# Performance work log

Hardware: AMD Instinct MI355X
Metric: run time of the kernel (lower is better)

Reference implementation:

```python
import jax, jax.numpy as jnp
import numpy as np

H = 16          # attention_head_num
DH = 64         # attention_head_size
D = H * DH      # out_dim / model dim
SIZE_PER_HEAD = 64  # scaling denominator (init arg, used as sqrt divisor)


def setup_inputs() -> dict:
    key = jax.random.key(0)
    ks = jax.random.split(key, 12)
    B, S = 2, 2048
    scale = 1.0 / np.sqrt(D)
    inp = {
        "qx": jax.random.normal(ks[0], (B, S, D), dtype=jnp.float32),
        "kx": jax.random.normal(ks[1], (B, S, D), dtype=jnp.float32),
        "vx": jax.random.normal(ks[2], (B, S, D), dtype=jnp.float32),
        "Wq": jax.random.normal(ks[3], (D, D), dtype=jnp.float32) * scale,
        "bq": jnp.zeros((D,), dtype=jnp.float32),
        "Wk": jax.random.normal(ks[4], (D, D), dtype=jnp.float32) * scale,
        "bk": jnp.zeros((D,), dtype=jnp.float32),
        "Wv": jax.random.normal(ks[5], (D, D), dtype=jnp.float32) * scale,
        "bv": jnp.zeros((D,), dtype=jnp.float32),
        "Wo": jax.random.normal(ks[6], (D, D), dtype=jnp.float32) * scale,
        "bo": jnp.zeros((D,), dtype=jnp.float32),
    }
    return inp


def reference(qx, kx, vx, Wq, bq, Wk, bk, Wv, bv, Wo, bo):
    B, Sq, _ = qx.shape
    Sk = kx.shape[1]
    # QKV projections
    q = qx @ Wq + bq  # [B,Sq,D]
    k = kx @ Wk + bk  # [B,Sk,D]
    v = vx @ Wv + bv  # [B,Sk,D]
    # split heads -> [B,H,S,DH]
    q = q.reshape(B, Sq, H, DH).transpose(0, 2, 1, 3)
    k = k.reshape(B, Sk, H, DH).transpose(0, 2, 1, 3)
    v = v.reshape(B, Sk, H, DH).transpose(0, 2, 1, 3)
    # scores [B,H,Sq,Sk]; NOTE: original divides by sqrt(size_per_head)
    scores = jnp.einsum("bhqd,bhkd->bhqk", q, k) / jnp.sqrt(
        jnp.asarray(SIZE_PER_HEAD, dtype=q.dtype)
    )
    probs = jax.nn.softmax(scores, axis=-1)
    ctx = jnp.einsum("bhqk,bhkd->bhqd", probs, v)  # [B,H,Sq,DH]
    ctx = ctx.transpose(0, 2, 1, 3).reshape(B, Sq, D)
    return ctx @ Wo + bo
```

## Files before the change

### kernel.cpp

```cpp
#include <hip/hip_runtime.h>

typedef _Float16 half_t;
typedef _Float16 half8 __attribute__((ext_vector_type(8)));
typedef float f32x16 __attribute__((ext_vector_type(16)));
typedef float f32x4v __attribute__((ext_vector_type(4)));

#define MFMA32(A, B, C) __builtin_amdgcn_mfma_f32_32x32x16_f16(A, B, C, 0, 0, 0)

#if __has_builtin(__builtin_amdgcn_exp2f)
#define EXP2F(x) __builtin_amdgcn_exp2f(x)
#else
#define EXP2F(x) exp2f(x)
#endif

static constexpr int S = 2048;
static constexpr int D = 1024;
static constexpr int H = 16;
static constexpr float QSCALE = 0.18033688011112042f;

__global__ __launch_bounds__(256) void cvt3(const float* __restrict__ x0, const float* __restrict__ x1,
                                            const float* __restrict__ x2,
                                            half_t* __restrict__ o0, half_t* __restrict__ o1,
                                            half_t* __restrict__ o2)
{
    int z = blockIdx.y;
    const float* s = (z == 0) ? x0 : (z == 1) ? x1 : x2;
    half_t* d = (z == 0) ? o0 : (z == 1) ? o1 : o2;
    size_t i = (size_t)blockIdx.x * 256 + threadIdx.x;
    const f32x4v* sp = (const f32x4v*)s;
    f32x4v a = sp[2 * i], b = sp[2 * i + 1];
    half8 h;
    h[0] = (half_t)a[0]; h[1] = (half_t)a[1]; h[2] = (half_t)a[2]; h[3] = (half_t)a[3];
    h[4] = (half_t)b[0]; h[5] = (half_t)b[1]; h[6] = (half_t)b[2]; h[7] = (half_t)b[3];
    *(half8*)(d + i * 8) = h;
}

__global__ __launch_bounds__(256) void wtrans(const float* __restrict__ w0, const float* __restrict__ w1,
                                              const float* __restrict__ w2, const float* __restrict__ w3,
                                              half_t* __restrict__ wt)
{
    __shared__ float tile[64][65];
    int z = blockIdx.y;
    const float* W = (z == 0) ? w0 : (z == 1) ? w1 : (z == 2) ? w2 : w3;
    half_t* out = wt + (size_t)z * D * D;
    int k0 = (blockIdx.x >> 4) * 64, n0 = (blockIdx.x & 15) * 64;
    int tid = threadIdx.x;
    int r = tid >> 4, c4 = (tid & 15) * 4;
#pragma unroll
    for (int p = 0; p < 4; ++p) {
        f32x4v v = *(const f32x4v*)(W + (size_t)(k0 + r + p * 16) * D + n0 + c4);
        tile[r + p * 16][c4 + 0] = v[0];
        tile[r + p * 16][c4 + 1] = v[1];
        tile[r + p * 16][c4 + 2] = v[2];
        tile[r + p * 16][c4 + 3] = v[3];
    }
    __syncthreads();
    int n = tid >> 3, kc = (tid & 7) * 8;
#pragma unroll
    for (int p = 0; p < 2; ++p) {
        int nn = n + p * 32;
        half8 h;
#pragma unroll
        for (int i = 0; i < 8; ++i) h[i] = (half_t)tile[kc + i][nn];
        *(half8*)(out + (size_t)(n0 + nn) * D + k0 + kc) = h;
    }
}

__global__ __launch_bounds__(256, 2) void gemm_qkv(
    const half_t* __restrict__ a0, const half_t* __restrict__ a1, const half_t* __restrict__ a2,
    const half_t* __restrict__ wt,
    const float* __restrict__ b0, const float* __restrict__ b1, const float* __restrict__ b2,
    half_t* __restrict__ qh, half_t* __restrict__ kh, half_t* __restrict__ vt)
{
    __shared__ half_t As[128 * 64];
    __shared__ half_t Bs[128 * 64];
    int z = blockIdx.z;
    const half_t* A = (z == 0) ? a0 : (z == 1) ? a1 : a2;
    const half_t* BT = wt + (size_t)z * D * D;
    const float* bias = (z == 0) ? b0 : (z == 1) ? b1 : b2;
    int m0 = (blockIdx.x >> 3) * 128, n0 = (blockIdx.x & 7) * 128;
    int tid = threadIdx.x, lane = tid & 63, wave = tid >> 6;
    int ml = lane & 31, hi = lane >> 5;
    int wm = (wave & 1) * 64, wn = (wave >> 1) * 64;
    int sr = tid >> 3, sc = tid & 7;

    f32x16 acc00 = {}, acc01 = {}, acc10 = {}, acc11 = {};

    for (int kk = 0; kk < D; kk += 64) {
        __syncthreads();
#pragma unroll
        for (int p = 0; p < 4; ++p) {
            int r = sr + p * 32;
            int sw = (sc ^ (r & 7)) * 8;
            *(half8*)(As + r * 64 + sw) = *(const half8*)(A + (size_t)(m0 + r) * D + kk + sc * 8);
            *(half8*)(Bs + r * 64 + sw) = *(const half8*)(BT + (size_t)(n0 + r) * D + kk + sc * 8);
        }
        __syncthreads();
        int rA0 = (wm + ml) * 64, rA1 = (wm + 32 + ml) * 64;
        int rB0 = (wn + ml) * 64, rB1 = (wn + 32 + ml) * 64;
#pragma unroll
        for (int ks = 0; ks < 4; ++ks) {
            int sw = ((ks * 2 + hi) ^ (ml & 7)) * 8;
            half8 af0 = *(const half8*)(As + rA0 + sw);
            half8 af1 = *(const half8*)(As + rA1 + sw);
            half8 bf0 = *(const half8*)(Bs + rB0 + sw);
            half8 bf1 = *(const half8*)(Bs + rB1 + sw);
            acc00 = MFMA32(af0, bf0, acc00);
            acc01 = MFMA32(af0, bf1, acc01);
            acc10 = MFMA32(af1, bf0, acc10);
            acc11 = MFMA32(af1, bf1, acc11);
        }
    }

#pragma unroll
    for (int nt = 0; nt < 2; ++nt) {
        int n = n0 + wn + nt * 32 + ml;
        float bv = bias[n];
#pragma unroll
        for (int mt = 0; mt < 2; ++mt) {
            f32x16 av = (mt == 0) ? (nt == 0 ? acc00 : acc01) : (nt == 0 ? acc10 : acc11);
            int rbase = m0 + wm + mt * 32 + 4 * hi;
#pragma unroll
            for (int r = 0; r < 16; ++r) {
                int row = rbase + (r & 3) + 8 * (r >> 2);
                float v = av[r] + bv;
                if (z == 0) {
                    qh[(size_t)row * D + n] = (half_t)(v * QSCALE);
                } else if (z == 1) {
                    kh[(size_t)row * D + n] = (half_t)v;
                } else {
                    int b = row >> 11, s = row & 2047, hh = n >> 6, dd = n & 63;
                    vt[(((size_t)(b * H + hh)) * 64 + dd) * S + s] = (half_t)v;
                }
            }
        }
    }
}

__global__ __launch_bounds__(256, 2) void gemm_out(
    const half_t* __restrict__ A, const half_t* __restrict__ BT,
    const float* __restrict__ bias, float* __restrict__ out)
{
    __shared__ half_t As[128 * 64];
    __shared__ half_t Bs[128 * 64];
    int m0 = (blockIdx.x >> 3) * 128, n0 = (blockIdx.x & 7) * 128;
    int tid = threadIdx.x, lane = tid & 63, wave = tid >> 6;
    int ml = lane & 31, hi = lane >> 5;
    int wm = (wave & 1) * 64, wn = (wave >> 1) * 64;
    int sr = tid >> 3, sc = tid & 7;

    f32x16 acc00 = {}, acc01 = {}, acc10 = {}, acc11 = {};

    for (int kk = 0; kk < D; kk += 64) {
        __syncthreads();
#pragma unroll
        for (int p = 0; p < 4; ++p) {
            int r = sr + p * 32;
            int sw = (sc ^ (r & 7)) * 8;
            *(half8*)(As + r * 64 + sw) = *(const half8*)(A + (size_t)(m0 + r) * D + kk + sc * 8);
            *(half8*)(Bs + r * 64 + sw) = *(const half8*)(BT + (size_t)(n0 + r) * D + kk + sc * 8);
        }
        __syncthreads();
        int rA0 = (wm + ml) * 64, rA1 = (wm + 32 + ml) * 64;
        int rB0 = (wn + ml) * 64, rB1 = (wn + 32 + ml) * 64;
#pragma unroll
        for (int ks = 0; ks < 4; ++ks) {
            int sw = ((ks * 2 + hi) ^ (ml & 7)) * 8;
            half8 af0 = *(const half8*)(As + rA0 + sw);
            half8 af1 = *(const half8*)(As + rA1 + sw);
            half8 bf0 = *(const half8*)(Bs + rB0 + sw);
            half8 bf1 = *(const half8*)(Bs + rB1 + sw);
            acc00 = MFMA32(af0, bf0, acc00);
            acc01 = MFMA32(af0, bf1, acc01);
            acc10 = MFMA32(af1, bf0, acc10);
            acc11 = MFMA32(af1, bf1, acc11);
        }
    }

#pragma unroll
    for (int nt = 0; nt < 2; ++nt) {
        int n = n0 + wn + nt * 32 + ml;
        float bv = bias[n];
#pragma unroll
        for (int mt = 0; mt < 2; ++mt) {
            f32x16 av = (mt == 0) ? (nt == 0 ? acc00 : acc01) : (nt == 0 ? acc10 : acc11);
            int rbase = m0 + wm + mt * 32 + 4 * hi;
#pragma unroll
            for (int r = 0; r < 16; ++r) {
                int row = rbase + (r & 3) + 8 * (r >> 2);
                out[(size_t)row * D + n] = av[r] + bv;
            }
        }
    }
}

__global__ __launch_bounds__(256, 2) void attn(
    const half_t* __restrict__ qh, const half_t* __restrict__ kh,
    const half_t* __restrict__ vt, half_t* __restrict__ ctx)
{
    __shared__ half_t Ks[128 * 64];
    __shared__ half_t VTs[64 * 128];
    __shared__ half_t Ps[4 * 32 * 128];
    int sq0 = blockIdx.x * 128, h = blockIdx.y, b = blockIdx.z;
    int tid = threadIdx.x, lane = tid & 63, wave = tid >> 6;
    int ml = lane & 31, hi = lane >> 5;
    size_t rowbase = (size_t)b * S;
    const half_t* vbase = vt + ((size_t)(b * H + h) * 64) * S;
    half_t* Pw = Ps + wave * (32 * 128);

    {
        int r = tid >> 3, c = tid & 7;
#pragma unroll
        for (int p = 0; p < 4; ++p) {
            int rr = r + p * 32;
            *(half8*)(Ks + rr * 64 + ((c ^ (rr & 7)) * 8)) =
                *(const half8*)(qh + (rowbase + sq0 + rr) * D + h * 64 + c * 8);
        }
    }
    __syncthreads();
    half8 qf[4];
    {
        int rq = (wave * 32 + ml) * 64;
#pragma unroll
        for (int ks = 0; ks < 4; ++ks)
            qf[ks] = *(const half8*)(Ks + rq + (((ks * 2 + hi) ^ (ml & 7)) * 8));
    }
    f32x16 oacc0 = {}, oacc1 = {}, lacc = {};
    half8 ones;
    {
        half_t ov = (ml == 0) ? (half_t)1.0f : (half_t)0.0f;
#pragma unroll
        for (int i = 0; i < 8; ++i) ones[i] = ov;
    }

    for (int sk0 = 0; sk0 < S; sk0 += 128) {
        __syncthreads();
        {
            int r = tid >> 3, c = tid & 7;
#pragma unroll
            for (int p = 0; p < 4; ++p) {
                int rr = r + p * 32;
                *(half8*)(Ks + rr * 64 + ((c ^ (rr & 7)) * 8)) =
                    *(const half8*)(kh + (rowbase + sk0 + rr) * D + h * 64 + c * 8);
            }
        }
        {
            int d = tid >> 4, c = tid & 15;
#pragma unroll
            for (int p = 0; p < 4; ++p) {
                int dd = d + p * 16;
                *(half8*)(VTs + dd * 128 + ((c ^ (dd & 7)) * 8)) =
                    *(const half8*)(vbase + (size_t)dd * S + sk0 + c * 8);
            }
        }
        __syncthreads();

        f32x16 sacc[4] = {};
#pragma unroll
        for (int ks = 0; ks < 4; ++ks) {
            int sw = ((ks * 2 + hi) ^ (ml & 7)) * 8;
            half8 kf0 = *(const half8*)(Ks + (ml)*64 + sw);
            half8 kf1 = *(const half8*)(Ks + (32 + ml) * 64 + sw);
            half8 kf2 = *(const half8*)(Ks + (64 + ml) * 64 + sw);
            half8 kf3 = *(const half8*)(Ks + (96 + ml) * 64 + sw);
            sacc[0] = MFMA32(qf[ks], kf0, sacc[0]);
            sacc[1] = MFMA32(qf[ks], kf1, sacc[1]);
            sacc[2] = MFMA32(qf[ks], kf2, sacc[2]);
            sacc[3] = MFMA32(qf[ks], kf3, sacc[3]);
        }

#pragma unroll
        for (int nt = 0; nt < 4; ++nt) {
            int kc = nt * 4 + (ml >> 3);
            int kj = ml & 7;
#pragma unroll
            for (int r = 0; r < 16; ++r) {
                int row = 4 * hi + (r & 3) + 8 * (r >> 2);
                float pv = EXP2F(sacc[nt][r] - 10.0f);
                Pw[row * 128 + ((kc ^ (row & 7)) * 8) + kj] = (half_t)pv;
            }
        }

#pragma unroll
        for (int ks = 0; ks < 8; ++ks) {
            int sw = ((ks * 2 + hi) ^ (ml & 7)) * 8;
            half8 pf = *(const half8*)(Pw + ml * 128 + sw);
            half8 vf0 = *(const half8*)(VTs + ml * 128 + sw);
            half8 vf1 = *(const half8*)(VTs + (32 + ml) * 128 + sw);
            oacc0 = MFMA32(pf, vf0, oacc0);
            oacc1 = MFMA32(pf, vf1, oacc1);
            lacc = MFMA32(pf, ones, lacc);
        }
    }

#pragma unroll
    for (int r = 0; r < 16; ++r) {
        float l = __shfl(lacc[r], lane & 32, 64);
        float linv = __builtin_amdgcn_rcpf(l);
        int row = wave * 32 + 4 * hi + (r & 3) + 8 * (r >> 2);
        size_t orow = (rowbase + sq0 + row) * D + h * 64;
        ctx[orow + ml] = (half_t)(oacc0[r] * linv);
        ctx[orow + 32 + ml] = (half_t)(oacc1[r] * linv);
    }
}

extern "C" void kernel_launch(void* const* d_in, const int* in_sizes, int n_in,
                              void* d_out, int out_size, void* d_ws, size_t ws_size,
                              hipStream_t stream)
{
    const float* qx = (const float*)d_in[0];
    const float* kx = (const float*)d_in[1];
    const float* vx = (const float*)d_in[2];
    const float* Wq = (const float*)d_in[3];
    const float* bq = (const float*)d_in[4];
    const float* Wk = (const float*)d_in[5];
    const float* bk = (const float*)d_in[6];
    const float* Wv = (const float*)d_in[7];
    const float* bv = (const float*)d_in[8];
    const float* Wo = (const float*)d_in[9];
    const float* bo = (const float*)d_in[10];
    float* out = (float*)d_out;

    half_t* ws = (half_t*)d_ws;
    const size_t NT = (size_t)4096 * 1024;
    half_t* qxh = ws;
    half_t* kxh = qxh + NT;
    half_t* vxh = kxh + NT;
    half_t* wt = vxh + NT;
    half_t* qh = wt + (size_t)4 * 1024 * 1024;
    half_t* kh = qh + NT;
    half_t* vtr = kh + NT;
    half_t* ctx = vtr + NT;

    cvt3<<<dim3(2048, 3), 256, 0, stream>>>(qx, kx, vx, qxh, kxh, vxh);
    wtrans<<<dim3(256, 4), 256, 0, stream>>>(Wq, Wk, Wv, Wo, wt);
    gemm_qkv<<<dim3(256, 1, 3), 256, 0, stream>>>(qxh, kxh, vxh, wt, bq, bk, bv, qh, kh, vtr);
    attn<<<dim3(16, 16, 2), 256, 0, stream>>>(qh, kh, vtr, ctx);
    gemm_out<<<dim3(256, 1, 1), 256, 0, stream>>>(ctx, wt + (size_t)3 * 1024 * 1024, bo, out);
}
```

Measured before the change: 256.3 us.

## Use direct global-to-LDS loads in GEMMs and restructure attention to keep P in registers

Both GEMMs now stage A/B tiles with global_load_lds into a column-chunk-major LDS layout, replacing register round-trip stores and XOR swizzle. The attention kernel is reworked: Q fragments come straight from global into registers, K/V tiles use direct LDS loads, and the P tile is permuted across lanes with shuffles instead of a round-trip through LDS. Waves split the key tile in halves and combine partial outputs and row sums through shared memory at the end. Row sums are accumulated in scalar registers instead of an extra MFMA against a ones vector. The attention grid is remapped to a 1D launch with a head-major block ordering. In exchange, the new unswizzled LDS layouts may cause bank conflicts, and the final cross-wave combine adds a shared-memory step.

Result: slower. 271.2 us (+5.8%).

```diff
diff --git a/kernel.cpp b/kernel.cpp
--- a/kernel.cpp
+++ b/kernel.cpp
@@ -2,6 +2,7 @@
 
 typedef _Float16 half_t;
 typedef _Float16 half8 __attribute__((ext_vector_type(8)));
+typedef _Float16 half2v __attribute__((ext_vector_type(2)));
 typedef float f32x16 __attribute__((ext_vector_type(16)));
 typedef float f32x4v __attribute__((ext_vector_type(4)));
 
@@ -17,6 +18,17 @@
 static constexpr int D = 1024;
 static constexpr int H = 16;
 static constexpr float QSCALE = 0.18033688011112042f;
+
+__device__ __forceinline__ void gload_lds16(const void* g, void* l) {
+    __builtin_amdgcn_global_load_lds(
+        (const __attribute__((address_space(1))) unsigned int*)g,
+        (__attribute__((address_space(3))) unsigned int*)l, 16, 0, 0);
+}
+
+__device__ __forceinline__ unsigned pk2(float a, float b) {
+    half2v h; h[0] = (half_t)a; h[1] = (half_t)b;
+    return __builtin_bit_cast(unsigned, h);
+}
 
 __global__ __launch_bounds__(256) void cvt3(const float* __restrict__ x0, const float* __restrict__ x1,
                                             const float* __restrict__ x2,
@@ -82,29 +94,28 @@
     int tid = threadIdx.x, lane = tid & 63, wave = tid >> 6;
     int ml = lane & 31, hi = lane >> 5;
     int wm = (wave & 1) * 64, wn = (wave >> 1) * 64;
-    int sr = tid >> 3, sc = tid & 7;
 
     f32x16 acc00 = {}, acc01 = {}, acc10 = {}, acc11 = {};
 
     for (int kk = 0; kk < D; kk += 64) {
         __syncthreads();
 #pragma unroll
-        for (int p = 0; p < 4; ++p) {
-            int r = sr + p * 32;
-            int sw = (sc ^ (r & 7)) * 8;
-            *(half8*)(As + r * 64 + sw) = *(const half8*)(A + (size_t)(m0 + r) * D + kk + sc * 8);
-            *(half8*)(Bs + r * 64 + sw) = *(const half8*)(BT + (size_t)(n0 + r) * D + kk + sc * 8);
-        }
-        __syncthreads();
-        int rA0 = (wm + ml) * 64, rA1 = (wm + 32 + ml) * 64;
-        int rB0 = (wn + ml) * 64, rB1 = (wn + 32 + ml) * 64;
+        for (int j = 0; j < 4; ++j) {
+            int idx = wave * 4 + j;
+            int c = idx >> 1, rh = idx & 1;
+            gload_lds16(A + (size_t)(m0 + rh * 64 + lane) * D + kk + c * 8,
+                        As + ((size_t)c * 128 + rh * 64) * 8);
+            gload_lds16(BT + (size_t)(n0 + rh * 64 + lane) * D + kk + c * 8,
+                        Bs + ((size_t)c * 128 + rh * 64) * 8);
+        }
+        __syncthreads();
 #pragma unroll
         for (int ks = 0; ks < 4; ++ks) {
-            int sw = ((ks * 2 + hi) ^ (ml & 7)) * 8;
-            half8 af0 = *(const half8*)(As + rA0 + sw);
-            half8 af1 = *(const half8*)(As + rA1 + sw);
-            half8 bf0 = *(const half8*)(Bs + rB0 + sw);
-            half8 bf1 = *(const half8*)(Bs + rB1 + sw);
+            int co = (2 * ks + hi) * 128;
+            half8 af0 = *(const half8*)(As + (size_t)(co + wm + ml) * 8);
+            half8 af1 = *(const half8*)(As + (size_t)(co + wm + 32 + ml) * 8);
+            half8 bf0 = *(const half8*)(Bs + (size_t)(co + wn + ml) * 8);
+            half8 bf1 = *(const half8*)(Bs + (size_t)(co + wn + 32 + ml) * 8);
             acc00 = MFMA32(af0, bf0, acc00);
             acc01 = MFMA32(af0, bf1, acc01);
             acc10 = MFMA32(af1, bf0, acc10);
@@ -147,29 +158,28 @@
     int tid = threadIdx.x, lane = tid & 63, wave = tid >> 6;
     int ml = lane & 31, hi = lane >> 5;
     int wm = (wave & 1) * 64, wn = (wave >> 1) * 64;
-    int sr = tid >> 3, sc = tid & 7;
 
     f32x16 acc00 = {}, acc01 = {}, acc10 = {}, acc11 = {};
 
     for (int kk = 0; kk < D; kk += 64) {
         __syncthreads();
 #pragma unroll
-        for (int p = 0; p < 4; ++p) {
-            int r = sr + p * 32;
-            int sw = (sc ^ (r & 7)) * 8;
-            *(half8*)(As + r * 64 + sw) = *(const half8*)(A + (size_t)(m0 + r) * D + kk + sc * 8);
-            *(half8*)(Bs + r * 64 + sw) = *(const half8*)(BT + (size_t)(n0 + r) * D + kk + sc * 8);
-        }
-        __syncthreads();
-        int rA0 = (wm + ml) * 64, rA1 = (wm + 32 + ml) * 64;
-        int rB0 = (wn + ml) * 64, rB1 = (wn + 32 + ml) * 64;
+        for (int j = 0; j < 4; ++j) {
+            int idx = wave * 4 + j;
+            int c = idx >> 1, rh = idx & 1;
+            gload_lds16(A + (size_t)(m0 + rh * 64 + lane) * D + kk + c * 8,
+                        As + ((size_t)c * 128 + rh * 64) * 8);
+            gload_lds16(BT + (size_t)(n0 + rh * 64 + lane) * D + kk + c * 8,
+                        Bs + ((size_t)c * 128 + rh * 64) * 8);
+        }
+        __syncthreads();
 #pragma unroll
         for (int ks = 0; ks < 4; ++ks) {
-            int sw = ((ks * 2 + hi) ^ (ml & 7)) * 8;
-            half8 af0 = *(const half8*)(As + rA0 + sw);
-            half8 af1 = *(const half8*)(As + rA1 + sw);
-            half8 bf0 = *(const half8*)(Bs + rB0 + sw);
-            half8 bf1 = *(const half8*)(Bs + rB1 + sw);
+            int co = (2 * ks + hi) * 128;
+            half8 af0 = *(const half8*)(As + (size_t)(co + wm + ml) * 8);
+            half8 af1 = *(const half8*)(As + (size_t)(co + wm + 32 + ml) * 8);
+            half8 bf0 = *(const half8*)(Bs + (size_t)(co + wn + ml) * 8);
+            half8 bf1 = *(const half8*)(Bs + (size_t)(co + wn + 32 + ml) * 8);
             acc00 = MFMA32(af0, bf0, acc00);
             acc01 = MFMA32(af0, bf1, acc01);
             acc10 = MFMA32(af1, bf0, acc10);
@@ -198,109 +208,128 @@
     const half_t* __restrict__ qh, const half_t* __restrict__ kh,
     const half_t* __restrict__ vt, half_t* __restrict__ ctx)
 {
-    __shared__ half_t Ks[128 * 64];
-    __shared__ half_t VTs[64 * 128];
-    __shared__ half_t Ps[4 * 32 * 128];
-    int sq0 = blockIdx.x * 128, h = blockIdx.y, b = blockIdx.z;
+    __shared__ char smem[33 * 1024];
+    half_t* Ks  = (half_t*)smem;
+    half_t* VTs = (half_t*)(smem + 16384);
+    float* Ocmb = (float*)smem;
+    float* Lcmb = (float*)(smem + 32768);
+
+    int L = blockIdx.x;
+    int slot = L >> 3;
+    int bh = (L & 7) + 8 * (slot >> 4);
+    int sq = slot & 15;
+    int b = bh >> 4, h = bh & 15;
+
     int tid = threadIdx.x, lane = tid & 63, wave = tid >> 6;
     int ml = lane & 31, hi = lane >> 5;
+    int qg = wave & 1, th = wave >> 1;
     size_t rowbase = (size_t)b * S;
-    const half_t* vbase = vt + ((size_t)(b * H + h) * 64) * S;
-    half_t* Pw = Ps + wave * (32 * 128);
-
+    const half_t* vbase = vt + (size_t)bh * 64 * S;
+    int sq0 = sq * 128;
+
+    half8 qf[2][4];
     {
-        int r = tid >> 3, c = tid & 7;
-#pragma unroll
-        for (int p = 0; p < 4; ++p) {
-            int rr = r + p * 32;
-            *(half8*)(Ks + rr * 64 + ((c ^ (rr & 7)) * 8)) =
-                *(const half8*)(qh + (rowbase + sq0 + rr) * D + h * 64 + c * 8);
-        }
-    }
+        const half_t* qrow = qh + (rowbase + sq0 + qg * 64 + ml) * (size_t)D + h * 64 + hi * 8;
+#pragma unroll
+        for (int qs = 0; qs < 2; ++qs)
+#pragma unroll
+            for (int ks = 0; ks < 4; ++ks)
+                qf[qs][ks] = *(const half8*)(qrow + (size_t)qs * 32 * D + ks * 16);
+    }
+
+    f32x16 oacc[2][2] = {};
+    float lsum[2] = {0.0f, 0.0f};
+
+    for (int it = 0; it < 16; ++it) {
+        int sk0 = it * 128;
+        __syncthreads();
+#pragma unroll
+        for (int j = 0; j < 4; ++j) {
+            int idx = wave * 4 + j;
+            int c = idx >> 1, rh = idx & 1;
+            gload_lds16(kh + (rowbase + sk0 + rh * 64 + lane) * (size_t)D + h * 64 + c * 8,
+                        Ks + ((size_t)c * 128 + rh * 64) * 8);
+            gload_lds16(vbase + (size_t)lane * S + sk0 + idx * 8,
+                        VTs + (size_t)idx * 64 * 8);
+        }
+        __syncthreads();
+
+#pragma unroll
+        for (int tt = 0; tt < 2; ++tt) {
+            int t = th * 2 + tt;
+            f32x16 s0 = {}, s1 = {};
+#pragma unroll
+            for (int ks = 0; ks < 4; ++ks) {
+                half8 kf = *(const half8*)(Ks + ((size_t)(2 * ks + hi) * 128 + t * 32 + ml) * 8);
+                s0 = MFMA32(kf, qf[0][ks], s0);
+                s1 = MFMA32(kf, qf[1][ks], s1);
+            }
+#pragma unroll
+            for (int qs = 0; qs < 2; ++qs) {
+                f32x16 sv = (qs == 0) ? s0 : s1;
+                float p[16];
+#pragma unroll
+                for (int r = 0; r < 16; ++r) {
+                    p[r] = EXP2F(sv[r] - 10.0f);
+                    lsum[qs] += p[r];
+                }
+                unsigned pkv[8];
+#pragma unroll
+                for (int j = 0; j < 8; ++j) pkv[j] = pk2(p[2 * j], p[2 * j + 1]);
+#pragma unroll
+                for (int kp = 0; kp < 2; ++kp) {
+                    unsigned e0 = pkv[4 * kp + 0], e1 = pkv[4 * kp + 1];
+                    unsigned o0 = pkv[4 * kp + 2], o1 = pkv[4 * kp + 3];
+                    unsigned s0u = hi ? e0 : o0, s1u = hi ? e1 : o1;
+                    unsigned k0u = hi ? o0 : e0, k1u = hi ? o1 : e1;
+                    unsigned r0 = __shfl_xor(s0u, 32, 64);
+                    unsigned r1 = __shfl_xor(s1u, 32, 64);
+                    union { unsigned u[4]; half8 h; } fr;
+                    fr.u[0] = hi ? r0 : k0u; fr.u[1] = hi ? r1 : k1u;
+                    fr.u[2] = hi ? k0u : r0; fr.u[3] = hi ? k1u : r1;
+#pragma unroll
+                    for (int dt = 0; dt < 2; ++dt) {
+                        half8 vf = *(const half8*)(VTs + ((size_t)(4 * t + 2 * kp + hi) * 64 + dt * 32 + ml) * 8);
+                        oacc[qs][dt] = MFMA32(fr.h, vf, oacc[qs][dt]);
+                    }
+                }
+            }
+        }
+    }
+
+    float lt[2];
+#pragma unroll
+    for (int qs = 0; qs < 2; ++qs) lt[qs] = lsum[qs] + __shfl_xor(lsum[qs], 32, 64);
     __syncthreads();
-    half8 qf[4];
-    {
-        int rq = (wave * 32 + ml) * 64;
-#pragma unroll
-        for (int ks = 0; ks < 4; ++ks)
-            qf[ks] = *(const half8*)(Ks + rq + (((ks * 2 + hi) ^ (ml & 7)) * 8));
-    }
-    f32x16 oacc0 = {}, oacc1 = {}, lacc = {};
-    half8 ones;
-    {
-        half_t ov = (ml == 0) ? (half_t)1.0f : (half_t)0.0f;
-#pragma unroll
-        for (int i = 0; i < 8; ++i) ones[i] = ov;
-    }
-
-    for (int sk0 = 0; sk0 < S; sk0 += 128) {
-        __syncthreads();
-        {
-            int r = tid >> 3, c = tid & 7;
-#pragma unroll
-            for (int p = 0; p < 4; ++p) {
-                int rr = r + p * 32;
-                *(half8*)(Ks + rr * 64 + ((c ^ (rr & 7)) * 8)) =
-                    *(const half8*)(kh + (rowbase + sk0 + rr) * D + h * 64 + c * 8);
-            }
-        }
-        {
-            int d = tid >> 4, c = tid & 15;
-#pragma unroll
-            for (int p = 0; p < 4; ++p) {
-                int dd = d + p * 16;
-                *(half8*)(VTs + dd * 128 + ((c ^ (dd & 7)) * 8)) =
-                    *(const half8*)(vbase + (size_t)dd * S + sk0 + c * 8);
-            }
-        }
-        __syncthreads();
-
-        f32x16 sacc[4] = {};
-#pragma unroll
-        for (int ks = 0; ks < 4; ++ks) {
-            int sw = ((ks * 2 + hi) ^ (ml & 7)) * 8;
-            half8 kf0 = *(const half8*)(Ks + (ml)*64 + sw);
-            half8 kf1 = *(const half8*)(Ks + (32 + ml) * 64 + sw);
-            half8 kf2 = *(const half8*)(Ks + (64 + ml) * 64 + sw);
-            half8 kf3 = *(const half8*)(Ks + (96 + ml) * 64 + sw);
-            sacc[0] = MFMA32(qf[ks], kf0, sacc[0]);
-            sacc[1] = MFMA32(qf[ks], kf1, sacc[1]);
-            sacc[2] = MFMA32(qf[ks], kf2, sacc[2]);
-            sacc[3] = MFMA32(qf[ks], kf3, sacc[3]);
-        }
-
-#pragma unroll
-        for (int nt = 0; nt < 4; ++nt) {
-            int kc = nt * 4 + (ml >> 3);
-            int kj = ml & 7;
-#pragma unroll
-            for (int r = 0; r < 16; ++r) {
-                int row = 4 * hi + (r & 3) + 8 * (r >> 2);
-                float pv = EXP2F(sacc[nt][r] - 10.0f);
-                Pw[row * 128 + ((kc ^ (row & 7)) * 8) + kj] = (half_t)pv;
-            }
-        }
-
-#pragma unroll
-        for (int ks = 0; ks < 8; ++ks) {
-            int sw = ((ks * 2 + hi) ^ (ml & 7)) * 8;
-            half8 pf = *(const half8*)(Pw + ml * 128 + sw);
-            half8 vf0 = *(const half8*)(VTs + ml * 128 + sw);
-            half8 vf1 = *(const half8*)(VTs + (32 + ml) * 128 + sw);
-            oacc0 = MFMA32(pf, vf0, oacc0);
-            oacc1 = MFMA32(pf, vf1, oacc1);
-            lacc = MFMA32(pf, ones, lacc);
-        }
-    }
-
-#pragma unroll
-    for (int r = 0; r < 16; ++r) {
-        float l = __shfl(lacc[r], lane & 32, 64);
-        float linv = __builtin_amdgcn_rcpf(l);
-        int row = wave * 32 + 4 * hi + (r & 3) + 8 * (r >> 2);
-        size_t orow = (rowbase + sq0 + row) * D + h * 64;
-        ctx[orow + ml] = (half_t)(oacc0[r] * linv);
-        ctx[orow + 32 + ml] = (half_t)(oacc1[r] * linv);
+    if (hi == 0) {
+        Lcmb[th * 128 + qg * 64 + ml] = lt[0];
+        Lcmb[th * 128 + qg * 64 + 32 + ml] = lt[1];
+    }
+    if (th == 1) {
+#pragma unroll
+        for (int qs = 0; qs < 2; ++qs)
+#pragma unroll
+            for (int dt = 0; dt < 2; ++dt)
+#pragma unroll
+                for (int r = 0; r < 16; ++r) {
+                    int q = qs * 32 + 4 * hi + (r & 3) + 8 * (r >> 2);
+                    Ocmb[(size_t)(qg * 64 + q) * 64 + dt * 32 + ml] = oacc[qs][dt][r];
+                }
+    }
+    __syncthreads();
+    if (th == 0) {
+#pragma unroll
+        for (int qs = 0; qs < 2; ++qs)
+#pragma unroll
+            for (int dt = 0; dt < 2; ++dt)
+#pragma unroll
+                for (int r = 0; r < 16; ++r) {
+                    int q = qs * 32 + 4 * hi + (r & 3) + 8 * (r >> 2);
+                    float l = Lcmb[qg * 64 + q] + Lcmb[128 + qg * 64 + q];
+                    float o = oacc[qs][dt][r] + Ocmb[(size_t)(qg * 64 + q) * 64 + dt * 32 + ml];
+                    ctx[(rowbase + sq0 + qg * 64 + q) * (size_t)D + h * 64 + dt * 32 + ml] =
+                        (half_t)(o * __builtin_amdgcn_rcpf(l));
+                }
     }
 }
 
@@ -335,6 +364,6 @@
     cvt3<<<dim3(2048, 3), 256, 0, stream>>>(qx, kx, vx, qxh, kxh, vxh);
     wtrans<<<dim3(256, 4), 256, 0, stream>>>(Wq, Wk, Wv, Wo, wt);
     gemm_qkv<<<dim3(256, 1, 3), 256, 0, stream>>>(qxh, kxh, vxh, wt, bq, bk, bv, qh, kh, vtr);
-    attn<<<dim3(16, 16, 2), 256, 0, stream>>>(qh, kh, vtr, ctx);
+    attn<<<dim3(512, 1, 1), 256, 0, stream>>>(qh, kh, vtr, ctx);
     gemm_out<<<dim3(256, 1, 1), 256, 0, stream>>>(ctx, wt + (size_t)3 * 1024 * 1024, bo, out);
 }
```
